# Kernel optimization log

Measured on AMD Instinct MI355X. Metric: run time of the kernel, lower is better.

The kernel has to match this reference:

```python
import jax, jax.numpy as jnp
import numpy as np

EPS = 1e-7  # K.epsilon()


def setup_inputs() -> dict:
    key = jax.random.key(0)
    k1, k2 = jax.random.split(key)
    B, T, D = 64, 4096, 256
    x = jax.random.normal(k1, (B, T, D), dtype=jnp.float32)
    W = jax.random.normal(k2, (D,), dtype=jnp.float32)
    b = jnp.zeros((T,), dtype=jnp.float32)
    return {"x": x, "W": W, "b": b}


def reference(x, W, b):
    # scores: [B, T] = x . W + b, then tanh
    eij = jnp.tanh(jnp.einsum('btd,d->bt', x, W) + b)
    a = jnp.exp(eij)
    a = a / (jnp.sum(a, axis=1, keepdims=True) + EPS)
    # weighted sum pooling over time: [B, D]
    return jnp.einsum('btd,bt->bd', x, a)
```

## Files before the change

### kernel.cpp

```cpp
#include <hip/hip_runtime.h>
#include <math.h>

#define B_  64
#define T_  4096
#define D_  256
#define BLOCKS_PER_B 16
#define T_PER_BLOCK  (T_ / BLOCKS_PER_B)
#define EPS 1e-7f

__global__ __launch_bounds__(256) void attn_pass1(
        const float* __restrict__ x,
        const float* __restrict__ W,
        const float* __restrict__ bias,
        float* __restrict__ partial) {
    const int blk  = blockIdx.x;
    const int b    = blk / BLOCKS_PER_B;
    const int tb   = blk % BLOCKS_PER_B;
    const int t0   = tb * T_PER_BLOCK;
    const int wave = threadIdx.x >> 6;
    const int lane = threadIdx.x & 63;

    const float4 wv = reinterpret_cast<const float4*>(W)[lane];

    float4 acc = make_float4(0.f, 0.f, 0.f, 0.f);
    float  S   = 0.f;

    const float4* xbase =
        reinterpret_cast<const float4*>(x + (size_t)b * T_ * D_);

    for (int t = t0 + wave; t < t0 + T_PER_BLOCK; t += 4) {
        float4 xv = xbase[(size_t)t * (D_ / 4) + lane];
        float dot = xv.x * wv.x + xv.y * wv.y + xv.z * wv.z + xv.w * wv.w;
        #pragma unroll
        for (int m = 1; m < 64; m <<= 1)
            dot += __shfl_xor(dot, m, 64);
        float a = expf(tanhf(dot + bias[t]));
        acc.x += a * xv.x;
        acc.y += a * xv.y;
        acc.z += a * xv.z;
        acc.w += a * xv.w;
        S += a;
    }

    __shared__ float sacc[4][D_];
    __shared__ float sS[4];
    reinterpret_cast<float4*>(&sacc[wave][0])[lane] = acc;
    if (lane == 0) sS[wave] = S;
    __syncthreads();

    const int d = threadIdx.x;
    float v = sacc[0][d] + sacc[1][d] + sacc[2][d] + sacc[3][d];
    float* p = partial + (size_t)blk * (D_ + 1);
    p[d] = v;
    if (d == 0) p[D_] = sS[0] + sS[1] + sS[2] + sS[3];
}

__global__ __launch_bounds__(256) void attn_pass2(
        const float* __restrict__ partial,
        float* __restrict__ out) {
    const int b = blockIdx.x;
    const int d = threadIdx.x;
    float acc = 0.f, S = 0.f;
    #pragma unroll
    for (int k = 0; k < BLOCKS_PER_B; ++k) {
        const float* p = partial + (size_t)(b * BLOCKS_PER_B + k) * (D_ + 1);
        acc += p[d];
        S   += p[D_];
    }
    out[b * D_ + d] = acc / (S + EPS);
}

extern "C" void kernel_launch(void* const* d_in, const int* in_sizes, int n_in,
                              void* d_out, int out_size, void* d_ws, size_t ws_size,
                              hipStream_t stream) {
    const float* x    = (const float*)d_in[0];
    const float* W    = (const float*)d_in[1];
    const float* bias = (const float*)d_in[2];
    float* out = (float*)d_out;
    float* partial = (float*)d_ws;

    attn_pass1<<<B_ * BLOCKS_PER_B, 256, 0, stream>>>(x, W, bias, partial);
    attn_pass2<<<B_, 256, 0, stream>>>(partial, out);
}
```

Measured before the change: 362.5 us.

## Unroll rows per wave with nontemporal loads, fast exp-tanh, and more blocks

Each wave now processes a contiguous chunk of rows, four at a time, issuing four independent nontemporal vector loads and interleaving their shuffle reductions. This exposes more memory-level parallelism and ILP. tanh+exp is replaced by a fast formulation built from __expf and a hardware reciprocal. The grid doubles to 32 blocks per batch, with a launch bound of 8 blocks per CU. Accuracy drops slightly from the approximate transcendental functions, and registers per thread go up.

```diff
diff --git a/kernel.cpp b/kernel.cpp
--- a/kernel.cpp
+++ b/kernel.cpp
@@ -4,11 +4,22 @@
 #define B_  64
 #define T_  4096
 #define D_  256
-#define BLOCKS_PER_B 16
+#define BLOCKS_PER_B 32
 #define T_PER_BLOCK  (T_ / BLOCKS_PER_B)
+#define WAVES_       4
+#define T_PER_WAVE   (T_PER_BLOCK / WAVES_)
+#define ROWS 4
 #define EPS 1e-7f
 
-__global__ __launch_bounds__(256) void attn_pass1(
+typedef float vfloat4 __attribute__((ext_vector_type(4)));
+
+__device__ __forceinline__ float exp_tanh(float s) {
+    float u = __expf(2.0f * s);
+    float t = 1.0f - 2.0f * __builtin_amdgcn_rcpf(u + 1.0f);
+    return __expf(t);
+}
+
+__global__ __launch_bounds__(256, 8) void attn_pass1(
         const float* __restrict__ x,
         const float* __restrict__ W,
         const float* __restrict__ bias,
@@ -16,35 +27,55 @@
     const int blk  = blockIdx.x;
     const int b    = blk / BLOCKS_PER_B;
     const int tb   = blk % BLOCKS_PER_B;
-    const int t0   = tb * T_PER_BLOCK;
     const int wave = threadIdx.x >> 6;
     const int lane = threadIdx.x & 63;
+    const int t0   = tb * T_PER_BLOCK + wave * T_PER_WAVE;
 
-    const float4 wv = reinterpret_cast<const float4*>(W)[lane];
+    const vfloat4 wv = reinterpret_cast<const vfloat4*>(W)[lane];
 
-    float4 acc = make_float4(0.f, 0.f, 0.f, 0.f);
-    float  S   = 0.f;
+    vfloat4 acc = (vfloat4)(0.f);
+    float   S   = 0.f;
 
-    const float4* xbase =
-        reinterpret_cast<const float4*>(x + (size_t)b * T_ * D_);
+    const vfloat4* xp = reinterpret_cast<const vfloat4*>(
+        x + (size_t)b * T_ * D_ + (size_t)t0 * D_) + lane;
 
-    for (int t = t0 + wave; t < t0 + T_PER_BLOCK; t += 4) {
-        float4 xv = xbase[(size_t)t * (D_ / 4) + lane];
-        float dot = xv.x * wv.x + xv.y * wv.y + xv.z * wv.z + xv.w * wv.w;
+    #pragma unroll 1
+    for (int i = 0; i < T_PER_WAVE; i += ROWS) {
+        vfloat4 xv0 = __builtin_nontemporal_load(&xp[0 * (D_ / 4)]);
+        vfloat4 xv1 = __builtin_nontemporal_load(&xp[1 * (D_ / 4)]);
+        vfloat4 xv2 = __builtin_nontemporal_load(&xp[2 * (D_ / 4)]);
+        vfloat4 xv3 = __builtin_nontemporal_load(&xp[3 * (D_ / 4)]);
+        xp += ROWS * (D_ / 4);
+
+        float d0 = fmaf(xv0.x, wv.x, fmaf(xv0.y, wv.y, fmaf(xv0.z, wv.z, xv0.w * wv.w)));
+        float d1 = fmaf(xv1.x, wv.x, fmaf(xv1.y, wv.y, fmaf(xv1.z, wv.z, xv1.w * wv.w)));
+        float d2 = fmaf(xv2.x, wv.x, fmaf(xv2.y, wv.y, fmaf(xv2.z, wv.z, xv2.w * wv.w)));
+        float d3 = fmaf(xv3.x, wv.x, fmaf(xv3.y, wv.y, fmaf(xv3.z, wv.z, xv3.w * wv.w)));
+
         #pragma unroll
-        for (int m = 1; m < 64; m <<= 1)
-            dot += __shfl_xor(dot, m, 64);
-        float a = expf(tanhf(dot + bias[t]));
-        acc.x += a * xv.x;
-        acc.y += a * xv.y;
-        acc.z += a * xv.z;
-        acc.w += a * xv.w;
-        S += a;
+        for (int m = 1; m < 64; m <<= 1) {
+            d0 += __shfl_xor(d0, m, 64);
+            d1 += __shfl_xor(d1, m, 64);
+            d2 += __shfl_xor(d2, m, 64);
+            d3 += __shfl_xor(d3, m, 64);
+        }
+
+        const int t = t0 + i;
+        float a0 = exp_tanh(d0 + bias[t + 0]);
+        float a1 = exp_tanh(d1 + bias[t + 1]);
+        float a2 = exp_tanh(d2 + bias[t + 2]);
+        float a3 = exp_tanh(d3 + bias[t + 3]);
+
+        acc.x += a0 * xv0.x + a1 * xv1.x + a2 * xv2.x + a3 * xv3.x;
+        acc.y += a0 * xv0.y + a1 * xv1.y + a2 * xv2.y + a3 * xv3.y;
+        acc.z += a0 * xv0.z + a1 * xv1.z + a2 * xv2.z + a3 * xv3.z;
+        acc.w += a0 * xv0.w + a1 * xv1.w + a2 * xv2.w + a3 * xv3.w;
+        S += a0 + a1 + a2 + a3;
     }
 
-    __shared__ float sacc[4][D_];
-    __shared__ float sS[4];
-    reinterpret_cast<float4*>(&sacc[wave][0])[lane] = acc;
+    __shared__ float sacc[WAVES_][D_];
+    __shared__ float sS[WAVES_];
+    reinterpret_cast<vfloat4*>(&sacc[wave][0])[lane] = acc;
     if (lane == 0) sS[wave] = S;
     __syncthreads();
 
```

Result: faster. 336.6 us (-7.1%).
